# Optimization experiments

Hardware: AMD Instinct MI355X
Metric: run time of the kernel (lower is better)

The kernel has to match this reference:

```python
import jax, jax.numpy as jnp
import numpy as np

N_NODES = 50000


def _gcn_norm(edge_index, n):
    # PyG GCNConv default: add self-loops, symmetric normalization.
    src = jnp.concatenate([edge_index[0], jnp.arange(n, dtype=edge_index.dtype)])
    dst = jnp.concatenate([edge_index[1], jnp.arange(n, dtype=edge_index.dtype)])
    deg = jax.ops.segment_sum(jnp.ones_like(dst, dtype=jnp.float32), dst, num_segments=n)
    dinv = jnp.where(deg > 0, jax.lax.rsqrt(deg), 0.0)
    norm = dinv[src] * dinv[dst]  # [E+N]
    return src, dst, norm


def _gcn_conv(x, src, dst, norm, W, b):
    h = x @ W                                   # dense transform [N, out]
    msg = norm[:, None] * h[src]                # gather + scale  [E+N, out]
    out = jax.ops.segment_sum(msg, dst, num_segments=x.shape[0])  # scatter-add
    return out + b


def setup_inputs() -> dict:
    key = jax.random.key(0)
    k1, k2, k3, k4, k5 = jax.random.split(key, 5)
    d_in, d_hid, n_cls = 128, 128, 2
    x = jax.random.normal(k1, (N_NODES, d_in), dtype=jnp.float32)
    edge_index = jax.random.randint(k2, (2, 600000), 0, N_NODES, dtype=jnp.int64)
    # Glorot-ish scaled params
    W1 = jax.random.normal(k3, (d_in, d_hid), dtype=jnp.float32) / np.sqrt(d_in)
    b1 = jnp.zeros((d_hid,), dtype=jnp.float32)
    W2 = jax.random.normal(k4, (d_hid, n_cls), dtype=jnp.float32) / np.sqrt(d_hid)
    b2 = jnp.zeros((n_cls,), dtype=jnp.float32)
    return {"x": x, "edge_index": edge_index, "W1": W1, "b1": b1, "W2": W2, "b2": b2}


def reference(x, edge_index, W1, b1, W2, b2):
    n = x.shape[0]
    src, dst, norm = _gcn_norm(edge_index, n)
    h = _gcn_conv(x, src, dst, norm, W1, b1)
    h = jax.nn.relu(h)
    # dropout omitted (eval mode / deterministic reference)
    out = _gcn_conv(h, src, dst, norm, W2, b2)
    return out
```

## Files before the change

### kernel.cpp

```cpp
#include <hip/hip_runtime.h>
#include <stdint.h>


#define D 128
#define CAP 64
#define NRT 3125
#define NT 8
#define GEMMB 391
#define FILLB 391
#define CSTRIDE 16

typedef short short8 __attribute__((ext_vector_type(8)));
typedef float f32x4 __attribute__((ext_vector_type(4)));

__device__ __forceinline__ float2 bf2_to_f2(unsigned int u) {
    float2 r;
    r.x = __uint_as_float(u << 16);
    r.y = __uint_as_float(u & 0xffff0000u);
    return r;
}
__device__ __forceinline__ unsigned short f2bf(float f) {
    unsigned int u = __float_as_uint(f);
    return (unsigned short)((u + 0x7fffu + ((u >> 16) & 1u)) >> 16);
}
__device__ __forceinline__ float bf2f(unsigned short s) {
    return __uint_as_float(((unsigned int)s) << 16);
}

__global__ __launch_bounds__(256) void zero_kernel(int4* __restrict__ p, int n4) {
    int i = blockIdx.x * 256 + threadIdx.x;
    if (i < n4) p[i] = make_int4(0, 0, 0, 0);
}

__global__ __launch_bounds__(256) void fill_gemm_kernel(
    const float* __restrict__ x, const int* __restrict__ ei,
    const float* __restrict__ W1,
    int* __restrict__ cntp, unsigned short* __restrict__ slots,
    unsigned short* __restrict__ h1u,
    int n, int E)
{
    const int tid = threadIdx.x;

    if (blockIdx.x & 1) {
        const int fb = blockIdx.x >> 1;
        for (int e = fb * 256 + tid; e < E; e += FILLB * 256) {
            int d = ei[E + e];
            int pos = atomicAdd(&cntp[(size_t)d * CSTRIDE], 1);
            if (pos < CAP) slots[(size_t)d * CAP + pos] = (unsigned short)ei[e];
        }
        return;
    }

    __shared__ unsigned short Ah[16 * 128];
    __shared__ unsigned short Al[16 * 128];

    const int wave = tid >> 6, lane = tid & 63;
    const int ln = lane & 15;
    const int kg = lane >> 4;
    const int cb = wave * 32;

    float wv[2][4][8];
#pragma unroll
    for (int ct = 0; ct < 2; ++ct)
#pragma unroll
        for (int ks = 0; ks < 4; ++ks)
#pragma unroll
            for (int j = 0; j < 8; ++j)
                wv[ct][ks][j] = W1[(size_t)(ks * 32 + kg * 8 + j) * D + cb + ct * 16 + ln];

    short8 bh[2][4], bl[2][4];
#pragma unroll
    for (int ct = 0; ct < 2; ++ct)
#pragma unroll
        for (int ks = 0; ks < 4; ++ks)
#pragma unroll
            for (int j = 0; j < 8; ++j) {
                float w = wv[ct][ks][j];
                unsigned short h = f2bf(w);
                bh[ct][ks][j] = (short)h;
                bl[ct][ks][j] = (short)f2bf(w - bf2f(h));
            }

    const int rt0 = (blockIdx.x >> 1) * NT;
    const int srow = tid >> 4;
    const int skb = (tid & 15) * 8;
    const int soff = ((srow * 128 + skb) ^ ((srow & 7) << 3));

    if (rt0 >= NRT) return;

    float4 pv0, pv1;
    {
        const float* xr = &x[(size_t)(rt0 * 16 + srow) * D + skb];
        pv0 = *(const float4*)xr;
        pv1 = *(const float4*)(xr + 4);
    }

    for (int it = 0; it < NT; ++it) {
        const int rt = rt0 + it;
        if (rt >= NRT) break;

        {
            const float f[8] = {pv0.x, pv0.y, pv0.z, pv0.w, pv1.x, pv1.y, pv1.z, pv1.w};
            short8 h8, l8;
#pragma unroll
            for (int j = 0; j < 8; ++j) {
                unsigned short h = f2bf(f[j]);
                h8[j] = (short)h;
                l8[j] = (short)f2bf(f[j] - bf2f(h));
            }
            *(short8*)&Ah[soff] = h8;
            *(short8*)&Al[soff] = l8;
        }
        __syncthreads();

        if (it + 1 < NT && rt + 1 < NRT) {
            const float* xr = &x[(size_t)((rt + 1) * 16 + srow) * D + skb];
            pv0 = *(const float4*)xr;
            pv1 = *(const float4*)(xr + 4);
        }

        f32x4 acc[2];
#pragma unroll
        for (int ct = 0; ct < 2; ++ct) acc[ct] = (f32x4){0.f, 0.f, 0.f, 0.f};
#pragma unroll
        for (int ks = 0; ks < 4; ++ks) {
            const int aoff = ((ln * 128 + ks * 32 + kg * 8) ^ ((ln & 7) << 3));
            short8 ah = *(const short8*)&Ah[aoff];
            short8 al = *(const short8*)&Al[aoff];
#pragma unroll
            for (int ct = 0; ct < 2; ++ct) {
                acc[ct] = __builtin_amdgcn_mfma_f32_16x16x32_bf16(ah, bh[ct][ks], acc[ct], 0, 0, 0);
                acc[ct] = __builtin_amdgcn_mfma_f32_16x16x32_bf16(al, bh[ct][ks], acc[ct], 0, 0, 0);
                acc[ct] = __builtin_amdgcn_mfma_f32_16x16x32_bf16(ah, bl[ct][ks], acc[ct], 0, 0, 0);
            }
        }
        __syncthreads();

        const int rowBase = rt * 16;
#pragma unroll
        for (int ct = 0; ct < 2; ++ct)
#pragma unroll
            for (int r = 0; r < 4; ++r) {
                int row = rowBase + kg * 4 + r;
                h1u[(size_t)row * D + cb + ct * 16 + ln] = f2bf(acc[ct][r]);
            }
    }
}

__global__ __launch_bounds__(256) void gather1_kernel(const int* __restrict__ cntp,
                                                      const unsigned short* __restrict__ slots,
                                                      const unsigned int* __restrict__ hs1b,
                                                      const float* __restrict__ b1,
                                                      const float* __restrict__ W2,
                                                      float* __restrict__ hs2, int n) {
    const int wave = threadIdx.x >> 6, lane = threadIdx.x & 63;
    const int i = blockIdx.x * 4 + wave;
    if (i >= n) return;

    const int ci = cntp[(size_t)i * CSTRIDE];
    const int m = min(ci, CAP);
    const float di = rsqrtf((float)ci + 1.0f);
    int idx = (lane < m) ? (int)slots[(size_t)i * CAP + lane] : 0;
    float dl = (lane < m) ? rsqrtf((float)cntp[(size_t)idx * CSTRIDE] + 1.0f) : 0.f;

    float2 h = bf2_to_f2(hs1b[(size_t)i * 64 + lane]);
    float ax0 = di * h.x, ay0 = di * h.y;
    float ax1 = 0.f, ay1 = 0.f;

    int j = 0;
    for (; j + 7 < m; j += 8) {
        int s[8];
        float dd[8];
#pragma unroll
        for (int q = 0; q < 8; ++q) {
            s[q] = __shfl(idx, j + q, 64);
            dd[q] = __shfl(dl, j + q, 64);
        }
        float2 v[8];
#pragma unroll
        for (int q = 0; q < 8; ++q) v[q] = bf2_to_f2(hs1b[(size_t)s[q] * 64 + lane]);
        ax0 = fmaf(dd[0], v[0].x, fmaf(dd[2], v[2].x, fmaf(dd[4], v[4].x, fmaf(dd[6], v[6].x, ax0))));
        ax1 = fmaf(dd[1], v[1].x, fmaf(dd[3], v[3].x, fmaf(dd[5], v[5].x, fmaf(dd[7], v[7].x, ax1))));
        ay0 = fmaf(dd[0], v[0].y, fmaf(dd[2], v[2].y, fmaf(dd[4], v[4].y, fmaf(dd[6], v[6].y, ay0))));
        ay1 = fmaf(dd[1], v[1].y, fmaf(dd[3], v[3].y, fmaf(dd[5], v[5].y, fmaf(dd[7], v[7].y, ay1))));
    }
    for (; j + 3 < m; j += 4) {
        int s[4];
        float dd[4];
#pragma unroll
        for (int q = 0; q < 4; ++q) {
            s[q] = __shfl(idx, j + q, 64);
            dd[q] = __shfl(dl, j + q, 64);
        }
        float2 v[4];
#pragma unroll
        for (int q = 0; q < 4; ++q) v[q] = bf2_to_f2(hs1b[(size_t)s[q] * 64 + lane]);
        ax0 = fmaf(dd[0], v[0].x, fmaf(dd[2], v[2].x, ax0));
        ax1 = fmaf(dd[1], v[1].x, fmaf(dd[3], v[3].x, ax1));
        ay0 = fmaf(dd[0], v[0].y, fmaf(dd[2], v[2].y, ay0));
        ay1 = fmaf(dd[1], v[1].y, fmaf(dd[3], v[3].y, ay1));
    }
    for (; j < m; ++j) {
        int s0 = __shfl(idx, j, 64);
        float d0 = __shfl(dl, j, 64);
        float2 v0 = bf2_to_f2(hs1b[(size_t)s0 * 64 + lane]);
        ax0 = fmaf(d0, v0.x, ax0);
        ay0 = fmaf(d0, v0.y, ay0);
    }
    float accx = ax0 + ax1, accy = ay0 + ay1;

    float2 b = *(const float2*)&b1[lane * 2];
    float hx = fmaxf(fmaf(di, accx, b.x), 0.f);
    float hy = fmaxf(fmaf(di, accy, b.y), 0.f);

    float4 w = *(const float4*)&W2[lane * 4];
    float p0 = fmaf(hx, w.x, hy * w.z);
    float p1 = fmaf(hx, w.y, hy * w.w);
#pragma unroll
    for (int off = 32; off > 0; off >>= 1) {
        p0 += __shfl_xor(p0, off, 64);
        p1 += __shfl_xor(p1, off, 64);
    }
    if (lane == 0) {
        hs2[2 * i + 0] = di * p0;
        hs2[2 * i + 1] = di * p1;
    }
}

__global__ __launch_bounds__(256) void gather2_kernel(const int* __restrict__ cntp,
                                                      const unsigned short* __restrict__ slots,
                                                      const float* __restrict__ hs2,
                                                      const float* __restrict__ b2,
                                                      float* __restrict__ out, int n) {
    int i = blockIdx.x * 256 + threadIdx.x;
    if (i >= n) return;
    const int ci = cntp[(size_t)i * CSTRIDE];
    const int m = min(ci, CAP);
    const unsigned short* sl = &slots[(size_t)i * CAP];
    float2 a = *(const float2*)&hs2[2 * i];
    float ax1 = 0.f, ay1 = 0.f;
    int e = 0;
    for (; e + 3 < m; e += 4) {
        int s0 = sl[e], s1 = sl[e + 1], s2 = sl[e + 2], s3 = sl[e + 3];
        float2 v0 = *(const float2*)&hs2[2 * s0];
        float2 v1 = *(const float2*)&hs2[2 * s1];
        float2 v2 = *(const float2*)&hs2[2 * s2];
        float2 v3 = *(const float2*)&hs2[2 * s3];
        a.x += v0.x + v2.x;
        ax1 += v1.x + v3.x;
        a.y += v0.y + v2.y;
        ay1 += v1.y + v3.y;
    }
    for (; e < m; ++e) {
        int s = sl[e];
        float2 v = *(const float2*)&hs2[2 * s];
        a.x += v.x;
        a.y += v.y;
    }
    a.x += ax1;
    a.y += ay1;
    float di = rsqrtf((float)ci + 1.0f);
    out[2 * i + 0] = fmaf(di, a.x, b2[0]);
    out[2 * i + 1] = fmaf(di, a.y, b2[1]);
}

extern "C" void kernel_launch(void* const* d_in, const int* in_sizes, int n_in,
                              void* d_out, int out_size, void* d_ws, size_t ws_size,
                              hipStream_t stream) {
    const float* x  = (const float*)d_in[0];
    const int*   ei = (const int*)d_in[1];
    const float* W1 = (const float*)d_in[2];
    const float* b1 = (const float*)d_in[3];
    const float* W2 = (const float*)d_in[4];
    const float* b2 = (const float*)d_in[5];

    const int n = in_sizes[0] / D;
    const int E = in_sizes[1] / 2;

    int* cntp             = (int*)d_ws;
    unsigned short* slots = (unsigned short*)(cntp + (size_t)n * CSTRIDE);
    unsigned int* hs1b    = (unsigned int*)(slots + (size_t)n * CAP);
    float* hs2            = (float*)(hs1b + (size_t)n * 64);
    float* out            = (float*)d_out;

    const int n4 = n * CSTRIDE / 4;

    zero_kernel<<<(n4 + 255) / 256, 256, 0, stream>>>((int4*)cntp, n4);
    fill_gemm_kernel<<<GEMMB + FILLB, 256, 0, stream>>>(
        x, ei, W1, cntp, slots, (unsigned short*)hs1b, n, E);
    gather1_kernel<<<(n + 3) / 4, 256, 0, stream>>>(cntp, slots, hs1b, b1, W2, hs2, n);
    gather2_kernel<<<(n + 255) / 256, 256, 0, stream>>>(cntp, slots, hs2, b2, out, n);
}
```

Baseline: 80.97 us.

## Privatize edge-bucket counters per XCD with workgroup-scope atomics and add merge step

The edge-fill phase now keeps a separate counter and slot array per XCD, read from the hardware XCC_ID register. It uses relaxed workgroup-scope atomics so contention stays in each XCD's L2 instead of going through device-scope atomics across dies. A new reduce kernel sums the per-XCD counts, and gather1 merges the per-XCD slot lists into a compact list through LDS, which gather2 then reuses. The block indexing of the fill and GEMM halves also changes so that fill blocks spread evenly over the XCDs. The cost is an extra kernel launch, more workspace, and a per-XCD cap of 16 that could drop edges for high-degree nodes. Correctness also relies on workgroup scope being coherent within one XCD's L2.

```diff
diff --git a/kernel.cpp b/kernel.cpp
--- a/kernel.cpp
+++ b/kernel.cpp
@@ -3,12 +3,13 @@
 
 
 #define D 128
-#define CAP 64
+#define CAP_S 16
+#define CAPC 64
 #define NRT 3125
 #define NT 8
-#define GEMMB 391
-#define FILLB 391
-#define CSTRIDE 16
+#define GRIDFG 784
+#define FILLB 392
+#define EPT_STRIDE (FILLB * 256)
 
 typedef short short8 __attribute__((ext_vector_type(8)));
 typedef float f32x4 __attribute__((ext_vector_type(4)));
@@ -35,18 +36,26 @@
 __global__ __launch_bounds__(256) void fill_gemm_kernel(
     const float* __restrict__ x, const int* __restrict__ ei,
     const float* __restrict__ W1,
-    int* __restrict__ cntp, unsigned short* __restrict__ slots,
+    int* __restrict__ cnt8, unsigned short* __restrict__ slots8,
     unsigned short* __restrict__ h1u,
     int n, int E)
 {
     const int tid = threadIdx.x;
-
-    if (blockIdx.x & 1) {
-        const int fb = blockIdx.x >> 1;
-        for (int e = fb * 256 + tid; e < E; e += FILLB * 256) {
+    const int bid = blockIdx.x;
+
+    if ((bid & 8) == 0) {
+        int xcd;
+        asm volatile("s_getreg_b32 %0, hwreg(HW_REG_XCC_ID)" : "=s"(xcd));
+        xcd &= 7;
+        const int f = (bid >> 4) * 8 + (bid & 7);
+        for (int e = f * 256 + tid; e < E; e += EPT_STRIDE) {
             int d = ei[E + e];
-            int pos = atomicAdd(&cntp[(size_t)d * CSTRIDE], 1);
-            if (pos < CAP) slots[(size_t)d * CAP + pos] = (unsigned short)ei[e];
+            size_t cell = (size_t)xcd * n + d;
+            int pos = __hip_atomic_fetch_add(&cnt8[cell], 1,
+                                             __ATOMIC_RELAXED,
+                                             __HIP_MEMORY_SCOPE_WORKGROUP);
+            if (pos < CAP_S)
+                slots8[cell * CAP_S + pos] = (unsigned short)ei[e];
         }
         return;
     }
@@ -81,7 +90,8 @@
                 bl[ct][ks][j] = (short)f2bf(w - bf2f(h));
             }
 
-    const int rt0 = (blockIdx.x >> 1) * NT;
+    const int g = (bid >> 4) * 8 + (bid & 7);
+    const int rt0 = g * NT;
     const int srow = tid >> 4;
     const int skb = (tid & 15) * 8;
     const int soff = ((srow * 128 + skb) ^ ((srow & 7) << 3));
@@ -147,21 +157,57 @@
     }
 }
 
-__global__ __launch_bounds__(256) void gather1_kernel(const int* __restrict__ cntp,
-                                                      const unsigned short* __restrict__ slots,
+__global__ __launch_bounds__(256) void reduce_kernel(const int* __restrict__ cnt8,
+                                                     int* __restrict__ cntc, int n) {
+    int i = blockIdx.x * 256 + threadIdx.x;
+    if (i >= n) return;
+    int s0 = min(cnt8[i], CAP_S)                  + min(cnt8[(size_t)n + i], CAP_S);
+    int s1 = min(cnt8[(size_t)2 * n + i], CAP_S)  + min(cnt8[(size_t)3 * n + i], CAP_S);
+    int s2 = min(cnt8[(size_t)4 * n + i], CAP_S)  + min(cnt8[(size_t)5 * n + i], CAP_S);
+    int s3 = min(cnt8[(size_t)6 * n + i], CAP_S)  + min(cnt8[(size_t)7 * n + i], CAP_S);
+    cntc[i] = (s0 + s1) + (s2 + s3);
+}
+
+__global__ __launch_bounds__(256) void gather1_kernel(const int* __restrict__ cnt8,
+                                                      const int* __restrict__ cntc,
+                                                      const unsigned short* __restrict__ slots8,
+                                                      unsigned short* __restrict__ slotsC,
                                                       const unsigned int* __restrict__ hs1b,
                                                       const float* __restrict__ b1,
                                                       const float* __restrict__ W2,
                                                       float* __restrict__ hs2, int n) {
+    __shared__ unsigned short lbuf[4][CAPC];
     const int wave = threadIdx.x >> 6, lane = threadIdx.x & 63;
     const int i = blockIdx.x * 4 + wave;
     if (i >= n) return;
 
-    const int ci = cntp[(size_t)i * CSTRIDE];
-    const int m = min(ci, CAP);
-    const float di = rsqrtf((float)ci + 1.0f);
-    int idx = (lane < m) ? (int)slots[(size_t)i * CAP + lane] : 0;
-    float dl = (lane < m) ? rsqrtf((float)cntp[(size_t)idx * CSTRIDE] + 1.0f) : 0.f;
+    int craw = 0;
+    if (lane < 8) craw = min(cnt8[(size_t)lane * n + i], CAP_S);
+    int c[8], base[8], b = 0;
+#pragma unroll
+    for (int s = 0; s < 8; ++s) {
+        c[s] = __shfl(craw, s, 64);
+        base[s] = b;
+        b += c[s];
+    }
+    const int m = min(b, CAPC);
+    const float di = rsqrtf((float)b + 1.0f);
+
+    {
+        int s = lane >> 3, k = lane & 7;
+        if (k < c[s]) {
+            int pos = base[s] + k;
+            if (pos < CAPC) lbuf[wave][pos] = slots8[((size_t)s * n + i) * CAP_S + k];
+        }
+        k += 8;
+        if (k < c[s]) {
+            int pos = base[s] + k;
+            if (pos < CAPC) lbuf[wave][pos] = slots8[((size_t)s * n + i) * CAP_S + k];
+        }
+    }
+    int idx = (lane < m) ? (int)lbuf[wave][lane] : 0;
+    if (lane < m) slotsC[(size_t)i * CAPC + lane] = (unsigned short)idx;
+    float dl = (lane < m) ? rsqrtf((float)cntc[idx] + 1.0f) : 0.f;
 
     float2 h = bf2_to_f2(hs1b[(size_t)i * 64 + lane]);
     float ax0 = di * h.x, ay0 = di * h.y;
@@ -209,9 +255,9 @@
     }
     float accx = ax0 + ax1, accy = ay0 + ay1;
 
-    float2 b = *(const float2*)&b1[lane * 2];
-    float hx = fmaxf(fmaf(di, accx, b.x), 0.f);
-    float hy = fmaxf(fmaf(di, accy, b.y), 0.f);
+    float2 bb = *(const float2*)&b1[lane * 2];
+    float hx = fmaxf(fmaf(di, accx, bb.x), 0.f);
+    float hy = fmaxf(fmaf(di, accy, bb.y), 0.f);
 
     float4 w = *(const float4*)&W2[lane * 4];
     float p0 = fmaf(hx, w.x, hy * w.z);
@@ -227,16 +273,16 @@
     }
 }
 
-__global__ __launch_bounds__(256) void gather2_kernel(const int* __restrict__ cntp,
-                                                      const unsigned short* __restrict__ slots,
+__global__ __launch_bounds__(256) void gather2_kernel(const int* __restrict__ cntc,
+                                                      const unsigned short* __restrict__ slotsC,
                                                       const float* __restrict__ hs2,
                                                       const float* __restrict__ b2,
                                                       float* __restrict__ out, int n) {
     int i = blockIdx.x * 256 + threadIdx.x;
     if (i >= n) return;
-    const int ci = cntp[(size_t)i * CSTRIDE];
-    const int m = min(ci, CAP);
-    const unsigned short* sl = &slots[(size_t)i * CAP];
+    const int ci = cntc[i];
+    const int m = min(ci, CAPC);
+    const unsigned short* sl = &slotsC[(size_t)i * CAPC];
     float2 a = *(const float2*)&hs2[2 * i];
     float ax1 = 0.f, ay1 = 0.f;
     int e = 0;
@@ -277,17 +323,21 @@
     const int n = in_sizes[0] / D;
     const int E = in_sizes[1] / 2;
 
-    int* cntp             = (int*)d_ws;
-    unsigned short* slots = (unsigned short*)(cntp + (size_t)n * CSTRIDE);
-    unsigned int* hs1b    = (unsigned int*)(slots + (size_t)n * CAP);
+    int* cnt8             = (int*)d_ws;
+    int* cntc             = cnt8 + (size_t)8 * n;
+    unsigned short* slotsC = (unsigned short*)(cntc + n);
+    unsigned short* slots8 = slotsC + (size_t)n * CAPC;
+    unsigned int* hs1b    = (unsigned int*)(slots8 + (size_t)8 * n * CAP_S);
     float* hs2            = (float*)(hs1b + (size_t)n * 64);
     float* out            = (float*)d_out;
 
-    const int n4 = n * CSTRIDE / 4;
-
-    zero_kernel<<<(n4 + 255) / 256, 256, 0, stream>>>((int4*)cntp, n4);
-    fill_gemm_kernel<<<GEMMB + FILLB, 256, 0, stream>>>(
-        x, ei, W1, cntp, slots, (unsigned short*)hs1b, n, E);
-    gather1_kernel<<<(n + 3) / 4, 256, 0, stream>>>(cntp, slots, hs1b, b1, W2, hs2, n);
-    gather2_kernel<<<(n + 255) / 256, 256, 0, stream>>>(cntp, slots, hs2, b2, out, n);
-}
+    const int n4 = 8 * n / 4;
+
+    zero_kernel<<<(n4 + 255) / 256, 256, 0, stream>>>((int4*)cnt8, n4);
+    fill_gemm_kernel<<<GRIDFG, 256, 0, stream>>>(
+        x, ei, W1, cnt8, slots8, (unsigned short*)hs1b, n, E);
+    reduce_kernel<<<(n + 255) / 256, 256, 0, stream>>>(cnt8, cntc, n);
+    gather1_kernel<<<(n + 3) / 4, 256, 0, stream>>>(
+        cnt8, cntc, slots8, slotsC, hs1b, b1, W2, hs2, n);
+    gather2_kernel<<<(n + 255) / 256, 256, 0, stream>>>(cntc, slotsC, hs2, b2, out, n);
+}
```

Result: slower. 86.56 us (+6.9%).
